# Optimization experiments

Hardware: AMD Instinct MI355X
Metric: run time of the kernel (lower is better)

The kernel has to match this reference:

```python
import jax, jax.numpy as jnp
import numpy as np

B, I, O, T, L, K, PAD = 16, 256, 256, 512, 8192, 7, 3
EPS = 1e-8


def setup_inputs() -> dict:
    key = jax.random.key(0)
    ks = jax.random.split(key, 7)
    bx = jax.random.normal(ks[0], (B, I, L), dtype=jnp.float32)
    t = jax.random.normal(ks[1], (B, T), dtype=jnp.float32)
    # depthwise conv weight: torch Conv1d(groups=I) weight is (I, 1, K)
    conv_w = jax.random.normal(ks[2], (I, 1, K), dtype=jnp.float32) * (1.0 / np.sqrt(K))
    # 1x1 proj: torch Conv1d weight (O, I, 1) -> store as (O, I)
    proj_w = jax.random.normal(ks[3], (O, I), dtype=jnp.float32) * (1.0 / np.sqrt(I))
    proj_b = jax.random.normal(ks[4], (O,), dtype=jnp.float32) * 0.01
    # Linear(t_dim -> in_dim)
    mod_w = jax.random.normal(ks[5], (I, T), dtype=jnp.float32) * (1.0 / np.sqrt(T))
    mod_b = jax.random.normal(ks[6], (I,), dtype=jnp.float32) * 0.01
    return {"bx": bx, "t": t, "conv_w": conv_w, "proj_w": proj_w,
            "proj_b": proj_b, "mod_w": mod_w, "mod_b": mod_b}


def reference(bx, t, conv_w, proj_w, proj_b, mod_w, mod_b):
    # modulation: (B, I)
    mod = t @ mod_w.T + mod_b
    # per-sample modulated 1x1 weights: (B, O, I)
    bw = proj_w[None, :, :] * (mod[:, None, :] + 1.0)
    # demodulation (L2 over input dim, kernel dim is size 1)
    demod = jax.lax.rsqrt(jnp.sum(bw * bw, axis=2) + EPS)  # (B, O)
    bw = bw * demod[:, :, None]
    # depthwise conv over length, 'same' padding (kernel 7, pad 3)
    xc = jax.lax.conv_general_dilated(
        bx, conv_w,
        window_strides=(1,), padding=[(PAD, PAD)],
        dimension_numbers=('NCH', 'OIH', 'NCH'),
        feature_group_count=I)  # (B, I, L)
    # per-sample grouped 1x1 conv == batched matmul
    out = jnp.einsum('boi,bil->bol', bw, xc) + proj_b[None, :, None]
    return out
```

## Files before the change

kernel.cpp:

```cpp
#include <hip/hip_runtime.h>
#include <hip/hip_bf16.h>

#define B_ 16
#define I_ 256
#define O_ 256
#define T_ 512
#define L_ 8192
#define K_ 7
#define PAD_ 3
#define BN 32
#define NTILE 256
#define LDK 264
#define XFS 39
#define XFN 2560

typedef unsigned short u16;
typedef unsigned int u32;
typedef __attribute__((ext_vector_type(8))) short short8;
typedef __attribute__((ext_vector_type(4))) float f32x4;

__device__ inline u16 f2bf(float f) {
    union { float f; u32 u; } v; v.f = f;
    u32 r = v.u + 0x7FFF + ((v.u >> 16) & 1);
    return (u16)(r >> 16);
}

__global__ void mod_kernel(const float* __restrict__ t, const float* __restrict__ mod_w,
                           const float* __restrict__ mod_b, float* __restrict__ mod) {
    int g = blockIdx.x, b = blockIdx.y;
    int lane = threadIdx.x & 63, wv = threadIdx.x >> 6;
    const float* tb = t + b * T_;
    #pragma unroll
    for (int q = 0; q < 4; ++q) {
        int i = g * 16 + wv * 4 + q;
        const float* wr = mod_w + (size_t)i * T_;
        float s = 0.f;
        #pragma unroll
        for (int u = 0; u < 8; ++u) s += wr[lane + u * 64] * tb[lane + u * 64];
        #pragma unroll
        for (int d = 32; d; d >>= 1) s += __shfl_down(s, d);
        if (lane == 0) mod[b * I_ + i] = s + mod_b[i];
    }
}

__global__ void wmod_kernel(const float* __restrict__ proj_w, const float* __restrict__ mod,
                            u16* __restrict__ Wb) {
    int og = blockIdx.x, b = blockIdx.y;
    int lane = threadIdx.x & 63, wv = threadIdx.x >> 6;
    const float* mrow = mod + b * I_;
    #pragma unroll
    for (int q = 0; q < 4; ++q) {
        int o = og * 16 + wv * 4 + q;
        const float* pw = proj_w + (size_t)o * I_;
        float4 pv = *(const float4*)(pw + lane * 4);
        float4 mv = *(const float4*)(mrow + lane * 4);
        float v0 = pv.x * (mv.x + 1.f);
        float v1 = pv.y * (mv.y + 1.f);
        float v2 = pv.z * (mv.z + 1.f);
        float v3 = pv.w * (mv.w + 1.f);
        float ss = v0*v0 + v1*v1 + v2*v2 + v3*v3;
        #pragma unroll
        for (int d = 32; d; d >>= 1) ss += __shfl_xor(ss, d);
        float dem = rsqrtf(ss + 1e-8f);
        u32 lo = (u32)f2bf(v0 * dem) | ((u32)f2bf(v1 * dem) << 16);
        u32 hi = (u32)f2bf(v2 * dem) | ((u32)f2bf(v3 * dem) << 16);
        *(uint2*)(Wb + (size_t)(b * O_ + o) * I_ + lane * 4) = make_uint2(lo, hi);
    }
}

__global__ __launch_bounds__(256, 4) void main_kernel(
    const float* __restrict__ bx, const float* __restrict__ conv_w,
    const u16* __restrict__ Wb, const float* __restrict__ proj_b,
    float* __restrict__ out)
{
    __shared__ __align__(16) float Xf[XFN];
    __shared__ __align__(16) u16 Xs[BN * LDK];

    const int tile = blockIdx.x;
    const int b = blockIdx.y;
    const int l0 = tile * BN;
    const int tid = threadIdx.x;
    const int lane = tid & 63;
    const int wv = tid >> 6;
    const int mlane = lane & 15;
    const int quad = lane >> 4;
    const float* bxr = bx + (size_t)b * I_ * L_;

    const int ch_init = tid / XFS;
    const int col_init = tid - ch_init * XFS;

    for (int ck = 0; ck < 4; ++ck) {
        const int ci0 = ck << 6;

        {
            int ch = ch_init, col = col_init;
            #pragma unroll
            for (int k = 0; k < 10; ++k) {
                int chc = ch < 63 ? ch : 63;
                int p = l0 - 4 + col;
                p = p < 0 ? 0 : (p > L_ - 1 ? L_ - 1 : p);
                const float* gp = bxr + (size_t)(ci0 + chc) * L_ + p;
                __builtin_amdgcn_global_load_lds(
                    (const __attribute__((address_space(1))) u32*)gp,
                    (__attribute__((address_space(3))) u32*)&Xf[k * 256 + tid], 4, 0, 0);
                ch += 6; col += 22;
                if (col >= XFS) { col -= XFS; ch += 1; }
            }
        }
        __syncthreads();

        if (tile == 0) {
            for (int z = tid; z < 64 * 4; z += 256)
                Xf[(z >> 2) * XFS + (z & 3)] = 0.f;
            __syncthreads();
        } else if (tile == NTILE - 1) {
            for (int z = tid; z < 64 * 3; z += 256) {
                int r = z / 3;
                Xf[r * XFS + 36 + (z - r * 3)] = 0.f;
            }
            __syncthreads();
        }

        {
            const int chl = tid & 63;
            const int s8 = (tid >> 6) << 3;
            const int ig = ci0 + chl;
            float w[K_];
            #pragma unroll
            for (int j = 0; j < K_; ++j) w[j] = conv_w[ig * K_ + j];
            const float* xr = &Xf[chl * XFS];
            float x[14];
            #pragma unroll
            for (int m = 0; m < 14; ++m) x[m] = xr[s8 + 1 + m];
            #pragma unroll
            for (int n = 0; n < 8; ++n) {
                float s = 0.f;
                #pragma unroll
                for (int j = 0; j < K_; ++j) s += w[j] * x[n + j];
                Xs[(s8 + n) * LDK + ig] = f2bf(s);
            }
        }
        __syncthreads();
    }

    f32x4 acc[4][2];
    #pragma unroll
    for (int r = 0; r < 4; ++r)
        #pragma unroll
        for (int c = 0; c < 2; ++c)
            acc[r][c] = (f32x4){0.f, 0.f, 0.f, 0.f};

    const u16* Wrow = Wb + (size_t)(b * O_ + wv * 64 + mlane) * I_;

    for (int kb = 0; kb < 8; ++kb) {
        const int koff = kb * 32 + quad * 8;
        short8 a[4], bbf[2];
        #pragma unroll
        for (int r = 0; r < 4; ++r)
            a[r] = *(const short8*)(Wrow + r * 16 * I_ + koff);
        #pragma unroll
        for (int c = 0; c < 2; ++c)
            bbf[c] = *(const short8*)(&Xs[(c * 16 + mlane) * LDK + koff]);
        #pragma unroll
        for (int r = 0; r < 4; ++r)
            #pragma unroll
            for (int c = 0; c < 2; ++c)
                acc[r][c] = __builtin_amdgcn_mfma_f32_16x16x32_bf16(a[r], bbf[c], acc[r][c], 0, 0, 0);
    }

    float* outb = out + (size_t)b * O_ * L_;
    #pragma unroll
    for (int r = 0; r < 4; ++r) {
        const int obase = wv * 64 + r * 16 + quad * 4;
        #pragma unroll
        for (int p = 0; p < 4; ++p) {
            const int o = obase + p;
            const float bias = proj_b[o];
            float* orow = outb + (size_t)o * L_ + l0 + mlane;
            #pragma unroll
            for (int c = 0; c < 2; ++c)
                orow[c * 16] = acc[r][c][p] + bias;
        }
    }
}

extern "C" void kernel_launch(void* const* d_in, const int* in_sizes, int n_in,
                              void* d_out, int out_size, void* d_ws, size_t ws_size,
                              hipStream_t stream) {
    const float* bx     = (const float*)d_in[0];
    const float* t      = (const float*)d_in[1];
    const float* conv_w = (const float*)d_in[2];
    const float* proj_w = (const float*)d_in[3];
    const float* proj_b = (const float*)d_in[4];
    const float* mod_w  = (const float*)d_in[5];
    const float* mod_b  = (const float*)d_in[6];
    float* out = (float*)d_out;

    float* mod = (float*)d_ws;
    u16*   Wb  = (u16*)((char*)d_ws + 16384);

    mod_kernel<<<dim3(16, 16), 256, 0, stream>>>(t, mod_w, mod_b, mod);
    wmod_kernel<<<dim3(16, 16), 256, 0, stream>>>(proj_w, mod, Wb);
    main_kernel<<<dim3(NTILE, 16), 256, 0, stream>>>(bx, conv_w, Wb, proj_b, out);
}
```

Before: 317.1 us.

## Double-buffer depthwise-conv input staging and prefetch next channel chunk

Stages the input tile into two shared-memory buffers so the global-to-LDS loads for the next 64-channel chunk are in flight while the current chunk's depthwise convolution runs. Waits use explicit vmcnt counts and raw barriers instead of __syncthreads. All conv weights are preloaded into registers up front, and boundary zero-padding is applied in registers rather than by extra LDS writes and barriers. This doubles the input LDS footprint and raises register pressure, which may reduce occupancy, and it relies on hand-counted vmcnt waits for correctness.

```diff
diff --git a/kernel.cpp b/kernel.cpp
--- a/kernel.cpp
+++ b/kernel.cpp
@@ -68,12 +68,27 @@
     }
 }
 
+#define STAGE(CI0, DST) do { \
+    int ch = ch_init, col = col_init; \
+    _Pragma("unroll") \
+    for (int k = 0; k < 10; ++k) { \
+        int chc = ch < 63 ? ch : 63; \
+        int p = l0 - 4 + col; \
+        p = p < 0 ? 0 : (p > L_ - 1 ? L_ - 1 : p); \
+        const float* gp = bxr + (size_t)((CI0) + chc) * L_ + p; \
+        __builtin_amdgcn_global_load_lds( \
+            (const __attribute__((address_space(1))) u32*)gp, \
+            (__attribute__((address_space(3))) u32*)&(DST)[k * 256 + tid], 4, 0, 0); \
+        ch += 6; col += 22; \
+        if (col >= XFS) { col -= XFS; ch += 1; } \
+    } } while (0)
+
 __global__ __launch_bounds__(256, 4) void main_kernel(
     const float* __restrict__ bx, const float* __restrict__ conv_w,
     const u16* __restrict__ Wb, const float* __restrict__ proj_b,
     float* __restrict__ out)
 {
-    __shared__ __align__(16) float Xf[XFN];
+    __shared__ __align__(16) float Xf[2][XFN];
     __shared__ __align__(16) u16 Xs[BN * LDK];
 
     const int tile = blockIdx.x;
@@ -88,59 +103,51 @@
 
     const int ch_init = tid / XFS;
     const int col_init = tid - ch_init * XFS;
-
+    const int chl = tid & 63;
+    const int s8v = (tid >> 6) << 3;
+
+    float wAll[4][K_];
+    #pragma unroll
+    for (int ck = 0; ck < 4; ++ck)
+        #pragma unroll
+        for (int j = 0; j < K_; ++j)
+            wAll[ck][j] = conv_w[((ck << 6) + chl) * K_ + j];
+    asm volatile("s_waitcnt vmcnt(0)" ::: "memory");
+
+    STAGE(0, Xf[0]);
+
+    #pragma unroll
     for (int ck = 0; ck < 4; ++ck) {
-        const int ci0 = ck << 6;
+        if (ck < 3) {
+            STAGE((ck + 1) << 6, Xf[(ck + 1) & 1]);
+            asm volatile("s_waitcnt vmcnt(10)" ::: "memory");
+        } else {
+            asm volatile("s_waitcnt vmcnt(0)" ::: "memory");
+        }
+        __builtin_amdgcn_sched_barrier(0);
+        __builtin_amdgcn_s_barrier();
+        __builtin_amdgcn_sched_barrier(0);
 
         {
-            int ch = ch_init, col = col_init;
-            #pragma unroll
-            for (int k = 0; k < 10; ++k) {
-                int chc = ch < 63 ? ch : 63;
-                int p = l0 - 4 + col;
-                p = p < 0 ? 0 : (p > L_ - 1 ? L_ - 1 : p);
-                const float* gp = bxr + (size_t)(ci0 + chc) * L_ + p;
-                __builtin_amdgcn_global_load_lds(
-                    (const __attribute__((address_space(1))) u32*)gp,
-                    (__attribute__((address_space(3))) u32*)&Xf[k * 256 + tid], 4, 0, 0);
-                ch += 6; col += 22;
-                if (col >= XFS) { col -= XFS; ch += 1; }
-            }
-        }
-        __syncthreads();
-
-        if (tile == 0) {
-            for (int z = tid; z < 64 * 4; z += 256)
-                Xf[(z >> 2) * XFS + (z & 3)] = 0.f;
-            __syncthreads();
-        } else if (tile == NTILE - 1) {
-            for (int z = tid; z < 64 * 3; z += 256) {
-                int r = z / 3;
-                Xf[r * XFS + 36 + (z - r * 3)] = 0.f;
-            }
-            __syncthreads();
-        }
-
-        {
-            const int chl = tid & 63;
-            const int s8 = (tid >> 6) << 3;
-            const int ig = ci0 + chl;
-            float w[K_];
-            #pragma unroll
-            for (int j = 0; j < K_; ++j) w[j] = conv_w[ig * K_ + j];
-            const float* xr = &Xf[chl * XFS];
+            const int ci0 = ck << 6;
+            const float* xr = &Xf[ck & 1][chl * XFS];
             float x[14];
             #pragma unroll
-            for (int m = 0; m < 14; ++m) x[m] = xr[s8 + 1 + m];
+            for (int m = 0; m < 14; ++m) x[m] = xr[s8v + 1 + m];
+            if (tile == 0 && s8v == 0)          { x[0] = 0.f; x[1] = 0.f; x[2] = 0.f; }
+            if (tile == NTILE - 1 && s8v == 24) { x[11] = 0.f; x[12] = 0.f; x[13] = 0.f; }
             #pragma unroll
             for (int n = 0; n < 8; ++n) {
                 float s = 0.f;
                 #pragma unroll
-                for (int j = 0; j < K_; ++j) s += w[j] * x[n + j];
-                Xs[(s8 + n) * LDK + ig] = f2bf(s);
+                for (int j = 0; j < K_; ++j) s += wAll[ck][j] * x[n + j];
+                Xs[(s8v + n) * LDK + (ci0 + chl)] = f2bf(s);
             }
         }
-        __syncthreads();
+        asm volatile("s_waitcnt lgkmcnt(0)" ::: "memory");
+        __builtin_amdgcn_sched_barrier(0);
+        __builtin_amdgcn_s_barrier();
+        __builtin_amdgcn_sched_barrier(0);
     }
 
     f32x4 acc[4][2];
```

Result: slower. 327.5 us (+3.3%).
